# Kernel optimization log

Measured on AMD Instinct MI355X. Metric: run time of the kernel, lower is better.

## Reference

```python
import jax, jax.numpy as jnp
import numpy as np

H, W = 256, 336
FLOW_SCALING = float(max(H, W))  # max(config['loader']['resolution'])
REG_WEIGHT = 0.001               # config['loss']['flow_regul_weight']
B, N = 8, 262144


def setup_inputs() -> dict:
    key = jax.random.key(0)
    k1, k2, k3, k4, k5 = jax.random.split(key, 5)
    # small flow so a reasonable fraction of warped events stays in-bounds
    flow = 0.05 * jax.random.normal(k1, (B, 2, H, W), dtype=jnp.float32)
    ys = jax.random.randint(k2, (B, N), 0, H).astype(jnp.float32)
    xs = jax.random.randint(k3, (B, N), 0, W).astype(jnp.float32)
    ts = jax.random.uniform(k4, (B, N), dtype=jnp.float32)  # normalized timestamps in [0,1]
    pol = jax.random.randint(k5, (B, N), 0, 2)
    # event layout per the code: (ts, y, x, p)
    event_list = jnp.stack([ts, ys, xs, pol.astype(jnp.float32) * 2.0 - 1.0], axis=-1)
    pol_mask = jnp.stack([(pol == 1), (pol == 0)], axis=-1).astype(jnp.float32)  # [B,N,2]
    return {"flow": flow, "event_list": event_list, "pol_mask": pol_mask}


def _get_interpolation(events, event_flow, tref):
    # warped event coords (y, x): [B, N, 2]
    warped = events[:, :, 1:3] + (tref - events[:, :, 0:1]) * event_flow * FLOW_SCALING
    top_y = jnp.floor(warped[:, :, 0:1])
    bot_y = jnp.floor(warped[:, :, 0:1] + 1.0)
    left_x = jnp.floor(warped[:, :, 1:2])
    right_x = jnp.floor(warped[:, :, 1:2] + 1.0)
    # four bilinear corners stacked along event dim -> [B, 4N, 2]
    idx = jnp.concatenate([
        jnp.concatenate([top_y, left_x], -1),
        jnp.concatenate([top_y, right_x], -1),
        jnp.concatenate([bot_y, left_x], -1),
        jnp.concatenate([bot_y, right_x], -1)], axis=1)
    warped4 = jnp.tile(warped, (1, 4, 1))
    weights = jnp.maximum(0.0, 1.0 - jnp.abs(warped4 - idx))
    mask = ((idx[:, :, 0:1] >= 0) & (idx[:, :, 0:1] < H)
            & (idx[:, :, 1:2] >= 0) & (idx[:, :, 1:2] < W)).astype(weights.dtype)
    idx = idx * mask          # unfeasible indices -> 0
    weights = weights * mask  # unfeasible weights -> 0
    flat_idx = (idx[:, :, 0] * W + idx[:, :, 1]).astype(jnp.int32)  # [B, 4N]
    w = jnp.prod(weights, axis=-1, keepdims=True)                    # [B, 4N, 1]
    return flat_idx, w


def _interpolate(flat_idx, weights, polarity_mask):
    # scatter-add bilinear weights into an H*W image, per batch element
    w = (weights * polarity_mask)[:, :, 0]  # [B, 4N]
    return jax.vmap(lambda i, v: jax.ops.segment_sum(v, i, num_segments=H * W))(flat_idx, w)


def reference(flow, event_list, pol_mask):
    pol4 = jnp.tile(pol_mask, (1, 4, 1))              # [B, 4N, 2]
    ts4 = jnp.tile(event_list[:, :, 0:1], (1, 4, 1))  # [B, 4N, 1]
    # gather flow at original event pixel locations
    flow_idx = (event_list[:, :, 1] * W + event_list[:, :, 2]).astype(jnp.int32)  # [B, N]
    flow_flat = flow.reshape(flow.shape[0], 2, -1)
    event_flowy = jnp.take_along_axis(flow_flat[:, 1, :], flow_idx, axis=1)
    event_flowx = jnp.take_along_axis(flow_flat[:, 0, :], flow_idx, axis=1)
    event_flow = jnp.stack([event_flowy, event_flowx], axis=-1)  # [B, N, 2] (y, x)

    loss = jnp.float32(0.0)
    # forward warp (tref=1, avg ts) and backward warp (tref=0, avg 1-ts)
    for tref, tgrad in ((1.0, ts4), (0.0, 1.0 - ts4)):
        idx, wts = _get_interpolation(event_list, event_flow, tref)
        for p in range(2):  # positive / negative polarity
            pm = pol4[:, :, p:p + 1]
            iwe = _interpolate(idx, wts, pm)
            iwe_ts = _interpolate(idx, wts * tgrad, pm)
            loss = loss + jnp.sum((iwe_ts / (iwe + 1e-9)) ** 2)

    # charbonnier flow smoothness
    flow_dx = flow[:, :, :-1, :] - flow[:, :, 1:, :]
    flow_dy = flow[:, :, :, :-1] - flow[:, :, :, 1:]
    smooth = jnp.sum(jnp.sqrt(flow_dx ** 2 + 1e-6)) + jnp.sum(jnp.sqrt(flow_dy ** 2 + 1e-6))
    return loss + REG_WEIGHT * smooth
```

## Files before the change

### kernel.cpp

```cpp
#include <hip/hip_runtime.h>

#define HH 256
#define WW 336
#define HWPIX (HH * WW)
#define BATCH 8
#define NEV 262144
#define NEV_SHIFT 18
#define FLOW_SCALING 336.0f
#define REG_WEIGHT 0.001f

#define BANDS 32
#define BANDSHIFT 3
#define BANDROWS 8
#define NBINS (2 * BATCH * BANDS)
#define CAP 14336
#define GSTRIDE 16

#define BE_THREADS 1024
#define EVPT 2
#define EV_PER_BLOCK (BE_THREADS * EVPT)
#define MAXITEMS 8320

#define HTILE (BANDROWS * WW)
#define NBLK_ACC NBINS

#define GCOUNT_BYTES (NBINS * GSTRIDE * 4)
#define ZERO_BYTES 33024
#define ITEMS_BYTES ((size_t)NBINS * CAP * 8)

__device__ __forceinline__ float wave_reduce_sum(float v) {
    #pragma unroll
    for (int o = 32; o > 0; o >>= 1) v += __shfl_down(v, o, 64);
    return v;
}

__device__ __forceinline__ float charb(float d) { return sqrtf(d * d + 1e-6f); }

__global__ __launch_bounds__(BE_THREADS)
void bin_events(const float* __restrict__ flow,
                const float4* __restrict__ ev,
                unsigned int* __restrict__ gcount,
                uint2* __restrict__ items) {
    __shared__ int lcnt[64];
    __shared__ int loff[64];
    __shared__ int gbase[64];
    __shared__ int stotal;
    __shared__ __align__(16) unsigned long long sval[MAXITEMS];

    int tid = threadIdx.x;
    if (tid < 64) lcnt[tid] = 0;
    __syncthreads();

    int base = blockIdx.x * EV_PER_BLOCK;
    int b = base >> NEV_SHIFT;
    const float* fxp = flow + (size_t)b * 2 * HWPIX;
    const float* fyp = fxp + HWPIX;

    unsigned int pkv[EVPT][2];
    unsigned int hiA[EVPT][2], hiB[EVPT][2];
    int rkA[EVPT][2], rkB[EVPT][2];

    #pragma unroll
    for (int e = 0; e < EVPT; ++e) {
        int bn = base + e * BE_THREADS + tid;
        float4 ee = ev[bn];
        float t = ee.x, y = ee.y, x = ee.z;
        unsigned int p = (ee.w > 0.0f) ? 0u : 1u;

        int iy = (int)y, ix = (int)x;
        int off = iy * WW + ix;
        float fx = fxp[off];
        float fy = fyp[off];

        #pragma unroll
        for (int tr = 0; tr < 2; ++tr) {
            rkA[e][tr] = -1; rkB[e][tr] = -1;
            float tref  = tr ? 0.0f : 1.0f;
            float tg    = tr ? (1.0f - t) : t;
            float dtS = (tref - t) * FLOW_SCALING;
            float wy = fmaf(dtS, fy, y);
            float wx = fmaf(dtS, fx, x);
            if (!(wx > -1.0f && wx < (float)WW)) continue;
            if (!(wy > -1.0f && wy < (float)HH)) continue;

            int ty = (int)floorf(wy);
            int band0 = -1, band1 = -1;
            if (ty >= 0 && ty < HH) band0 = ty >> BANDSHIFT;
            int r1 = ty + 1;
            if (r1 >= 0 && r1 < HH) {
                int bb = r1 >> BANDSHIFT;
                if (bb != band0) band1 = bb;
            }

            unsigned int qx = (unsigned int)(fmaf(wx, 2048.0f, 2048.5f));
            unsigned int qt = (unsigned int)(tg * 2047.0f + 0.5f);
            pkv[e][tr] = (qx << 12) | (qt << 1) | p;

            if (band0 >= 0) {
                float wyrel = wy - (float)(band0 * BANDROWS - 1);
                unsigned int qy = (unsigned int)fmaf(wyrel, 2048.0f, 0.5f);
                int lb = tr * BANDS + band0;
                hiA[e][tr] = qy | ((unsigned int)lb << 16);
                rkA[e][tr] = atomicAdd(&lcnt[lb], 1);
            }
            if (band1 >= 0) {
                float wyrel = wy - (float)(band1 * BANDROWS - 1);
                unsigned int qy = (unsigned int)fmaf(wyrel, 2048.0f, 0.5f);
                int lb = tr * BANDS + band1;
                hiB[e][tr] = qy | ((unsigned int)lb << 16);
                rkB[e][tr] = atomicAdd(&lcnt[lb], 1);
            }
        }
    }
    __syncthreads();

    if (tid < 64) {
        int c  = lcnt[tid];
        int ce = (c + 1) & ~1;
        int xg = ce;
        #pragma unroll
        for (int o = 1; o < 64; o <<= 1) {
            int yv = __shfl_up(xg, o, 64);
            if (tid >= o) xg += yv;
        }
        int lo = xg - ce;
        loff[tid] = lo;
        if (tid == 63) stotal = xg;
        int gbin = ((tid >> 5) * BATCH + b) * BANDS + (tid & 31);
        gbase[tid] = ce > 0 ? (int)atomicAdd(&gcount[gbin * GSTRIDE],
                                             (unsigned int)ce) : 0;
        if (c & 1) {
            unsigned int hi = (15u << 11) | ((unsigned int)tid << 16);
            sval[lo + c] = ((unsigned long long)hi << 32);
        }
    }
    __syncthreads();

    #pragma unroll
    for (int e = 0; e < EVPT; ++e) {
        #pragma unroll
        for (int tr = 0; tr < 2; ++tr) {
            if (rkA[e][tr] >= 0) {
                int lb = (hiA[e][tr] >> 16) & 63;
                sval[loff[lb] + rkA[e][tr]] =
                    (unsigned long long)pkv[e][tr] |
                    ((unsigned long long)hiA[e][tr] << 32);
            }
            if (rkB[e][tr] >= 0) {
                int lb = (hiB[e][tr] >> 16) & 63;
                sval[loff[lb] + rkB[e][tr]] =
                    (unsigned long long)pkv[e][tr] |
                    ((unsigned long long)hiB[e][tr] << 32);
            }
        }
    }
    __syncthreads();

    int total = stotal;
    for (int i = tid * 2; i < total; i += 2 * BE_THREADS) {
        uint4 two = *(const uint4*)&sval[i];
        unsigned int pk0 = two.x, h0 = two.y;
        unsigned int qy0 = h0 & 0xffffu;
        int lb0 = (h0 >> 16) & 63;
        int gs0 = gbase[lb0] + (i - loff[lb0]);
        int gbin0 = ((lb0 >> 5) * BATCH + b) * BANDS + (lb0 & 31);

        if ((i + 1) < total) {
            unsigned int pk1 = two.z, h1 = two.w;
            unsigned int qy1 = h1 & 0xffffu;
            int lb1 = (h1 >> 16) & 63;
            int gs1 = gbase[lb1] + (i + 1 - loff[lb1]);
            if (lb1 == lb0 && (gs0 & 1) == 0 && gs1 < CAP) {
                *(uint4*)(items + (size_t)gbin0 * CAP + gs0) =
                    make_uint4(pk0, qy0, pk1, qy1);
                continue;
            }
            int gbin1 = ((lb1 >> 5) * BATCH + b) * BANDS + (lb1 & 31);
            if (gs1 < CAP) items[(size_t)gbin1 * CAP + gs1] = make_uint2(pk1, qy1);
        }
        if (gs0 < CAP) items[(size_t)gbin0 * CAP + gs0] = make_uint2(pk0, qy0);
    }
}

__device__ __forceinline__ unsigned int pack_w(float w, float tg) {
    unsigned int lo16 = (unsigned int)fmaf(w, 1024.0f, 0.5f);
    unsigned int hi16 = (unsigned int)fmaf(w * tg, 1024.0f, 0.5f);
    return lo16 | (hi16 << 16);
}

__device__ __forceinline__ void accum_item(unsigned int* __restrict__ sA,
                                           unsigned int* __restrict__ sB,
                                           unsigned int pk, unsigned int qy) {
    float wx = (float)(pk >> 12) * (1.0f / 2048.0f) - 1.0f;
    float tg = (float)((pk >> 1) & 2047u) * (1.0f / 2047.0f);
    int p = pk & 1u;

    int rowq = qy >> 11;
    float fy = (float)(qy & 2047u) * (1.0f / 2048.0f);
    int row_top = rowq - 1;

    float lxf = floorf(wx);
    float fxx = wx - lxf;
    int lx = (int)lxf;

    unsigned int* A  = sA + p * HTILE;
    unsigned int* Bb = sB + p * HTILE;

    #pragma unroll
    for (int a = 0; a < 2; ++a) {
        int ry = row_top + a;
        if ((unsigned)ry >= (unsigned)BANDROWS) continue;
        float wrow = a ? fy : (1.0f - fy);
        int rb = ry * WW;
        if (lx >= 0 && lx + 1 < WW) {
            unsigned int pl = pack_w(wrow * (1.0f - fxx), tg);
            unsigned int pr = pack_w(wrow * fxx, tg);
            unsigned long long v =
                (unsigned long long)pl | ((unsigned long long)pr << 32);
            if ((lx & 1) == 0) {
                atomicAdd((unsigned long long*)(A + rb + lx), v);
            } else {
                atomicAdd((unsigned long long*)(Bb + rb + lx - 1), v);
            }
        } else if (lx == -1) {
            atomicAdd(&A[rb], pack_w(wrow * fxx, tg));
        } else if (lx == WW - 1) {
            atomicAdd(&A[rb + lx], pack_w(wrow * (1.0f - fxx), tg));
        }
    }
}

__global__ __launch_bounds__(1024)
void bin_accum(const float* __restrict__ flow,
               const unsigned int* __restrict__ gcount,
               const uint2* __restrict__ items,
               float* __restrict__ loss_acc,
               unsigned int* __restrict__ done_count,
               float* __restrict__ out) {
    __shared__ __align__(16) unsigned int sA[2 * HTILE];
    __shared__ __align__(16) unsigned int sB[2 * HTILE];
    __shared__ float red[16];
    __shared__ int lastflag;

    int band = blockIdx.x;
    int tr   = blockIdx.y;
    int b    = blockIdx.z;
    int tid  = threadIdx.x;
    int lblk = band + 32 * (tr + 2 * b);

    for (int i = tid; i < 2 * HTILE; i += 1024) { sA[i] = 0u; sB[i] = 0u; }
    __syncthreads();

    int gbin = (tr * BATCH + b) * BANDS + band;
    int cnt = min((int)gcount[gbin * GSTRIDE], CAP);
    const uint2* bp = items + (size_t)gbin * CAP;
    const uint4* bp4 = (const uint4*)bp;

    int nquad = cnt >> 2;
    if (tid < nquad) {
        uint4 c0 = bp4[2 * tid];
        uint4 c1 = bp4[2 * tid + 1];
        for (int n = tid + 1024; n < nquad; n += 1024) {
            uint4 d0 = bp4[2 * n];
            uint4 d1 = bp4[2 * n + 1];
            accum_item(sA, sB, c0.x, c0.y);
            accum_item(sA, sB, c0.z, c0.w);
            accum_item(sA, sB, c1.x, c1.y);
            accum_item(sA, sB, c1.z, c1.w);
            c0 = d0; c1 = d1;
        }
        accum_item(sA, sB, c0.x, c0.y);
        accum_item(sA, sB, c0.z, c0.w);
        accum_item(sA, sB, c1.x, c1.y);
        accum_item(sA, sB, c1.z, c1.w);
    }
    int rem = cnt & 3;
    if (tid < rem) {
        uint2 u = bp[nquad * 4 + tid];
        accum_item(sA, sB, u.x, u.y);
    }

    float sm = 0.0f;
    {
        const int N4 = BATCH * HWPIX / 4;
        const int H4 = HWPIX / 4;
        const int W4 = WW / 4;
        for (int i = lblk * 1024 + tid; i < N4; i += NBLK_ACC * 1024) {
            int bb = i / H4, u = i - bb * H4;
            int row = u / W4, c4 = u - row * W4;
            const float4* ch0 = (const float4*)(flow + (size_t)bb * 2 * HWPIX);
            const float4* ch1 = ch0 + H4;
            float4 a0 = ch0[u];
            float4 a1 = ch1[u];
            if (row < HH - 1) {
                float4 d0 = ch0[u + W4];
                float4 d1 = ch1[u + W4];
                sm += charb(a0.x - d0.x) + charb(a0.y - d0.y) +
                      charb(a0.z - d0.z) + charb(a0.w - d0.w) +
                      charb(a1.x - d1.x) + charb(a1.y - d1.y) +
                      charb(a1.z - d1.z) + charb(a1.w - d1.w);
            }
            sm += charb(a0.x - a0.y) + charb(a0.y - a0.z) + charb(a0.z - a0.w) +
                  charb(a1.x - a1.y) + charb(a1.y - a1.z) + charb(a1.z - a1.w);
            if (c4 < W4 - 1) {
                float r0 = ((const float*)ch0)[4 * u + 4];
                float r1 = ((const float*)ch1)[4 * u + 4];
                sm += charb(a0.w - r0) + charb(a1.w - r1);
            }
        }
    }
    __syncthreads();

    float v = 0.0f;
    for (int i = tid; i < 2 * HTILE; i += 1024) {
        int px = i - (i / WW) * WW;
        unsigned int u = sA[i] + (px ? sB[i - 1] : 0u);
        float iwe = (float)(u & 0xffffu);
        float its = (float)(u >> 16);
        float r = its / (iwe + 1.024e-6f);
        v += r * r;
    }
    v = fmaf(sm, REG_WEIGHT, v);
    v = wave_reduce_sum(v);
    if ((tid & 63) == 0) red[tid >> 6] = v;
    __syncthreads();
    if (tid == 0) {
        float r = 0.0f;
        #pragma unroll
        for (int k = 0; k < 16; ++k) r += red[k];
        atomicAdd(loss_acc, r);
        __threadfence();
        unsigned int t = atomicAdd(done_count, 1u);
        lastflag = (t == (unsigned)(NBLK_ACC - 1));
    }
    __syncthreads();

    if (lastflag && tid == 0) {
        *out = atomicAdd(loss_acc, 0.0f);
    }
}

extern "C" void kernel_launch(void* const* d_in, const int* in_sizes, int n_in,
                              void* d_out, int out_size, void* d_ws, size_t ws_size,
                              hipStream_t stream) {
    const float*  flow  = (const float*)d_in[0];
    const float4* ev    = (const float4*)d_in[1];
    float* out = (float*)d_out;

    unsigned int* gcount     = (unsigned int*)d_ws;
    float*        loss_acc   = (float*)((char*)d_ws + GCOUNT_BYTES);
    unsigned int* done_count = (unsigned int*)((char*)d_ws + GCOUNT_BYTES + 4);
    uint2*        items      = (uint2*)((char*)d_ws + GCOUNT_BYTES + 4096);

    hipMemsetAsync(d_ws, 0, ZERO_BYTES, stream);

    int total_ev = BATCH * NEV;
    bin_events<<<total_ev / EV_PER_BLOCK, BE_THREADS, 0, stream>>>(
        flow, ev, gcount, items);

    dim3 g2(BANDS, 2, BATCH);
    bin_accum<<<g2, 1024, 0, stream>>>(flow, gcount, items, loss_acc,
                                       done_count, out);
}
```

Before: 138.3 us.

## Replace band binning with direct global atomic scatter into per-plane accumulators

Drops the two-pass scheme that binned events into row bands and accumulated them in shared memory. Each event now does packed 64-bit atomic adds straight into full-image global accumulator planes, and a separate grid-stride kernel reduces the loss and smoothness term. This removes the binning, prefix-scan and item staging traffic. In exchange it adds a memset of two roughly 11 MB accumulators and relies on global atomics in L2, which have higher latency and can contend where events collide.

```diff
diff --git a/kernel.cpp b/kernel.cpp
--- a/kernel.cpp
+++ b/kernel.cpp
@@ -9,24 +9,18 @@
 #define FLOW_SCALING 336.0f
 #define REG_WEIGHT 0.001f
 
-#define BANDS 32
-#define BANDSHIFT 3
-#define BANDROWS 8
-#define NBINS (2 * BATCH * BANDS)
-#define CAP 14336
-#define GSTRIDE 16
-
-#define BE_THREADS 1024
+#define NPLANE (BATCH * 2 * 2)
+#define ACC_U32 (NPLANE * HWPIX)
+#define ACC_BYTES ((size_t)ACC_U32 * 4)
+
+#define WS_THREADS 1024
 #define EVPT 2
-#define EV_PER_BLOCK (BE_THREADS * EVPT)
-#define MAXITEMS 8320
-
-#define HTILE (BANDROWS * WW)
-#define NBLK_ACC NBINS
-
-#define GCOUNT_BYTES (NBINS * GSTRIDE * 4)
-#define ZERO_BYTES 33024
-#define ITEMS_BYTES ((size_t)NBINS * CAP * 8)
+#define EV_PER_BLOCK (WS_THREADS * EVPT)
+
+#define RL_BLOCKS 512
+#define RL_THREADS 1024
+
+#define ZERO_BYTES (2 * ACC_BYTES + 64)
 
 __device__ __forceinline__ float wave_reduce_sum(float v) {
     #pragma unroll
@@ -36,248 +30,106 @@
 
 __device__ __forceinline__ float charb(float d) { return sqrtf(d * d + 1e-6f); }
 
-__global__ __launch_bounds__(BE_THREADS)
-void bin_events(const float* __restrict__ flow,
-                const float4* __restrict__ ev,
-                unsigned int* __restrict__ gcount,
-                uint2* __restrict__ items) {
-    __shared__ int lcnt[64];
-    __shared__ int loff[64];
-    __shared__ int gbase[64];
-    __shared__ int stotal;
-    __shared__ __align__(16) unsigned long long sval[MAXITEMS];
-
+__device__ __forceinline__ unsigned int pack_w(float w, float tg) {
+    unsigned int lo16 = (unsigned int)fmaf(w, 1024.0f, 0.5f);
+    unsigned int hi16 = (unsigned int)fmaf(w * tg, 1024.0f, 0.5f);
+    return lo16 | (hi16 << 16);
+}
+
+__device__ __forceinline__ void scatter_ev(unsigned int* __restrict__ A,
+                                           unsigned int* __restrict__ B,
+                                           const float* __restrict__ fxp,
+                                           const float* __restrict__ fyp,
+                                           float4 e, int b) {
+    float t = e.x, y = e.y, x = e.z;
+    unsigned int p = (e.w > 0.0f) ? 0u : 1u;
+
+    int off = (int)y * WW + (int)x;
+    float fx = fxp[off];
+    float fy = fyp[off];
+
+    #pragma unroll
+    for (int tr = 0; tr < 2; ++tr) {
+        float tref = tr ? 0.0f : 1.0f;
+        float tg   = tr ? (1.0f - t) : t;
+        float dtS  = (tref - t) * FLOW_SCALING;
+        float wy = fmaf(dtS, fy, y);
+        float wx = fmaf(dtS, fx, x);
+        if (!(wx > -1.0f && wx < (float)WW)) continue;
+        if (!(wy > -1.0f && wy < (float)HH)) continue;
+
+        float tyf = floorf(wy);
+        float lxf = floorf(wx);
+        float fyy = wy - tyf;
+        float fxx = wx - lxf;
+        int ty = (int)tyf;
+        int lx = (int)lxf;
+
+        int pbase = (((b << 1) | tr) << 1 | (int)p) * HWPIX;
+
+        #pragma unroll
+        for (int a = 0; a < 2; ++a) {
+            int ry = ty + a;
+            if ((unsigned)ry >= (unsigned)HH) continue;
+            float wrow = a ? fyy : (1.0f - fyy);
+            int rb = pbase + ry * WW;
+            if (lx >= 0 && lx + 1 < WW) {
+                unsigned int pl = pack_w(wrow * (1.0f - fxx), tg);
+                unsigned int pr = pack_w(wrow * fxx, tg);
+                unsigned long long v =
+                    (unsigned long long)pl | ((unsigned long long)pr << 32);
+                if ((lx & 1) == 0) {
+                    atomicAdd((unsigned long long*)(A + rb + lx), v);
+                } else {
+                    atomicAdd((unsigned long long*)(B + rb + lx - 1), v);
+                }
+            } else if (lx == -1) {
+                atomicAdd(&A[rb], pack_w(wrow * fxx, tg));
+            } else if (lx == WW - 1) {
+                atomicAdd(&A[rb + lx], pack_w(wrow * (1.0f - fxx), tg));
+            }
+        }
+    }
+}
+
+__global__ __launch_bounds__(WS_THREADS)
+void warp_scatter(const float* __restrict__ flow,
+                  const float4* __restrict__ ev,
+                  unsigned int* __restrict__ A,
+                  unsigned int* __restrict__ B) {
     int tid = threadIdx.x;
-    if (tid < 64) lcnt[tid] = 0;
-    __syncthreads();
-
     int base = blockIdx.x * EV_PER_BLOCK;
     int b = base >> NEV_SHIFT;
     const float* fxp = flow + (size_t)b * 2 * HWPIX;
     const float* fyp = fxp + HWPIX;
 
-    unsigned int pkv[EVPT][2];
-    unsigned int hiA[EVPT][2], hiB[EVPT][2];
-    int rkA[EVPT][2], rkB[EVPT][2];
-
-    #pragma unroll
-    for (int e = 0; e < EVPT; ++e) {
-        int bn = base + e * BE_THREADS + tid;
-        float4 ee = ev[bn];
-        float t = ee.x, y = ee.y, x = ee.z;
-        unsigned int p = (ee.w > 0.0f) ? 0u : 1u;
-
-        int iy = (int)y, ix = (int)x;
-        int off = iy * WW + ix;
-        float fx = fxp[off];
-        float fy = fyp[off];
-
-        #pragma unroll
-        for (int tr = 0; tr < 2; ++tr) {
-            rkA[e][tr] = -1; rkB[e][tr] = -1;
-            float tref  = tr ? 0.0f : 1.0f;
-            float tg    = tr ? (1.0f - t) : t;
-            float dtS = (tref - t) * FLOW_SCALING;
-            float wy = fmaf(dtS, fy, y);
-            float wx = fmaf(dtS, fx, x);
-            if (!(wx > -1.0f && wx < (float)WW)) continue;
-            if (!(wy > -1.0f && wy < (float)HH)) continue;
-
-            int ty = (int)floorf(wy);
-            int band0 = -1, band1 = -1;
-            if (ty >= 0 && ty < HH) band0 = ty >> BANDSHIFT;
-            int r1 = ty + 1;
-            if (r1 >= 0 && r1 < HH) {
-                int bb = r1 >> BANDSHIFT;
-                if (bb != band0) band1 = bb;
-            }
-
-            unsigned int qx = (unsigned int)(fmaf(wx, 2048.0f, 2048.5f));
-            unsigned int qt = (unsigned int)(tg * 2047.0f + 0.5f);
-            pkv[e][tr] = (qx << 12) | (qt << 1) | p;
-
-            if (band0 >= 0) {
-                float wyrel = wy - (float)(band0 * BANDROWS - 1);
-                unsigned int qy = (unsigned int)fmaf(wyrel, 2048.0f, 0.5f);
-                int lb = tr * BANDS + band0;
-                hiA[e][tr] = qy | ((unsigned int)lb << 16);
-                rkA[e][tr] = atomicAdd(&lcnt[lb], 1);
-            }
-            if (band1 >= 0) {
-                float wyrel = wy - (float)(band1 * BANDROWS - 1);
-                unsigned int qy = (unsigned int)fmaf(wyrel, 2048.0f, 0.5f);
-                int lb = tr * BANDS + band1;
-                hiB[e][tr] = qy | ((unsigned int)lb << 16);
-                rkB[e][tr] = atomicAdd(&lcnt[lb], 1);
-            }
-        }
-    }
-    __syncthreads();
-
-    if (tid < 64) {
-        int c  = lcnt[tid];
-        int ce = (c + 1) & ~1;
-        int xg = ce;
-        #pragma unroll
-        for (int o = 1; o < 64; o <<= 1) {
-            int yv = __shfl_up(xg, o, 64);
-            if (tid >= o) xg += yv;
-        }
-        int lo = xg - ce;
-        loff[tid] = lo;
-        if (tid == 63) stotal = xg;
-        int gbin = ((tid >> 5) * BATCH + b) * BANDS + (tid & 31);
-        gbase[tid] = ce > 0 ? (int)atomicAdd(&gcount[gbin * GSTRIDE],
-                                             (unsigned int)ce) : 0;
-        if (c & 1) {
-            unsigned int hi = (15u << 11) | ((unsigned int)tid << 16);
-            sval[lo + c] = ((unsigned long long)hi << 32);
-        }
-    }
-    __syncthreads();
-
-    #pragma unroll
-    for (int e = 0; e < EVPT; ++e) {
-        #pragma unroll
-        for (int tr = 0; tr < 2; ++tr) {
-            if (rkA[e][tr] >= 0) {
-                int lb = (hiA[e][tr] >> 16) & 63;
-                sval[loff[lb] + rkA[e][tr]] =
-                    (unsigned long long)pkv[e][tr] |
-                    ((unsigned long long)hiA[e][tr] << 32);
-            }
-            if (rkB[e][tr] >= 0) {
-                int lb = (hiB[e][tr] >> 16) & 63;
-                sval[loff[lb] + rkB[e][tr]] =
-                    (unsigned long long)pkv[e][tr] |
-                    ((unsigned long long)hiB[e][tr] << 32);
-            }
-        }
-    }
-    __syncthreads();
-
-    int total = stotal;
-    for (int i = tid * 2; i < total; i += 2 * BE_THREADS) {
-        uint4 two = *(const uint4*)&sval[i];
-        unsigned int pk0 = two.x, h0 = two.y;
-        unsigned int qy0 = h0 & 0xffffu;
-        int lb0 = (h0 >> 16) & 63;
-        int gs0 = gbase[lb0] + (i - loff[lb0]);
-        int gbin0 = ((lb0 >> 5) * BATCH + b) * BANDS + (lb0 & 31);
-
-        if ((i + 1) < total) {
-            unsigned int pk1 = two.z, h1 = two.w;
-            unsigned int qy1 = h1 & 0xffffu;
-            int lb1 = (h1 >> 16) & 63;
-            int gs1 = gbase[lb1] + (i + 1 - loff[lb1]);
-            if (lb1 == lb0 && (gs0 & 1) == 0 && gs1 < CAP) {
-                *(uint4*)(items + (size_t)gbin0 * CAP + gs0) =
-                    make_uint4(pk0, qy0, pk1, qy1);
-                continue;
-            }
-            int gbin1 = ((lb1 >> 5) * BATCH + b) * BANDS + (lb1 & 31);
-            if (gs1 < CAP) items[(size_t)gbin1 * CAP + gs1] = make_uint2(pk1, qy1);
-        }
-        if (gs0 < CAP) items[(size_t)gbin0 * CAP + gs0] = make_uint2(pk0, qy0);
-    }
-}
-
-__device__ __forceinline__ unsigned int pack_w(float w, float tg) {
-    unsigned int lo16 = (unsigned int)fmaf(w, 1024.0f, 0.5f);
-    unsigned int hi16 = (unsigned int)fmaf(w * tg, 1024.0f, 0.5f);
-    return lo16 | (hi16 << 16);
-}
-
-__device__ __forceinline__ void accum_item(unsigned int* __restrict__ sA,
-                                           unsigned int* __restrict__ sB,
-                                           unsigned int pk, unsigned int qy) {
-    float wx = (float)(pk >> 12) * (1.0f / 2048.0f) - 1.0f;
-    float tg = (float)((pk >> 1) & 2047u) * (1.0f / 2047.0f);
-    int p = pk & 1u;
-
-    int rowq = qy >> 11;
-    float fy = (float)(qy & 2047u) * (1.0f / 2048.0f);
-    int row_top = rowq - 1;
-
-    float lxf = floorf(wx);
-    float fxx = wx - lxf;
-    int lx = (int)lxf;
-
-    unsigned int* A  = sA + p * HTILE;
-    unsigned int* Bb = sB + p * HTILE;
-
-    #pragma unroll
-    for (int a = 0; a < 2; ++a) {
-        int ry = row_top + a;
-        if ((unsigned)ry >= (unsigned)BANDROWS) continue;
-        float wrow = a ? fy : (1.0f - fy);
-        int rb = ry * WW;
-        if (lx >= 0 && lx + 1 < WW) {
-            unsigned int pl = pack_w(wrow * (1.0f - fxx), tg);
-            unsigned int pr = pack_w(wrow * fxx, tg);
-            unsigned long long v =
-                (unsigned long long)pl | ((unsigned long long)pr << 32);
-            if ((lx & 1) == 0) {
-                atomicAdd((unsigned long long*)(A + rb + lx), v);
-            } else {
-                atomicAdd((unsigned long long*)(Bb + rb + lx - 1), v);
-            }
-        } else if (lx == -1) {
-            atomicAdd(&A[rb], pack_w(wrow * fxx, tg));
-        } else if (lx == WW - 1) {
-            atomicAdd(&A[rb + lx], pack_w(wrow * (1.0f - fxx), tg));
-        }
-    }
-}
-
-__global__ __launch_bounds__(1024)
-void bin_accum(const float* __restrict__ flow,
-               const unsigned int* __restrict__ gcount,
-               const uint2* __restrict__ items,
-               float* __restrict__ loss_acc,
-               unsigned int* __restrict__ done_count,
-               float* __restrict__ out) {
-    __shared__ __align__(16) unsigned int sA[2 * HTILE];
-    __shared__ __align__(16) unsigned int sB[2 * HTILE];
+    float4 e0 = ev[base + tid];
+    float4 e1 = ev[base + WS_THREADS + tid];
+
+    scatter_ev(A, B, fxp, fyp, e0, b);
+    scatter_ev(A, B, fxp, fyp, e1, b);
+}
+
+__global__ __launch_bounds__(RL_THREADS)
+void reduce_loss(const unsigned int* __restrict__ A,
+                 const unsigned int* __restrict__ B,
+                 const float* __restrict__ flow,
+                 float* __restrict__ loss_acc,
+                 unsigned int* __restrict__ done_count,
+                 float* __restrict__ out) {
     __shared__ float red[16];
     __shared__ int lastflag;
-
-    int band = blockIdx.x;
-    int tr   = blockIdx.y;
-    int b    = blockIdx.z;
-    int tid  = threadIdx.x;
-    int lblk = band + 32 * (tr + 2 * b);
-
-    for (int i = tid; i < 2 * HTILE; i += 1024) { sA[i] = 0u; sB[i] = 0u; }
-    __syncthreads();
-
-    int gbin = (tr * BATCH + b) * BANDS + band;
-    int cnt = min((int)gcount[gbin * GSTRIDE], CAP);
-    const uint2* bp = items + (size_t)gbin * CAP;
-    const uint4* bp4 = (const uint4*)bp;
-
-    int nquad = cnt >> 2;
-    if (tid < nquad) {
-        uint4 c0 = bp4[2 * tid];
-        uint4 c1 = bp4[2 * tid + 1];
-        for (int n = tid + 1024; n < nquad; n += 1024) {
-            uint4 d0 = bp4[2 * n];
-            uint4 d1 = bp4[2 * n + 1];
-            accum_item(sA, sB, c0.x, c0.y);
-            accum_item(sA, sB, c0.z, c0.w);
-            accum_item(sA, sB, c1.x, c1.y);
-            accum_item(sA, sB, c1.z, c1.w);
-            c0 = d0; c1 = d1;
-        }
-        accum_item(sA, sB, c0.x, c0.y);
-        accum_item(sA, sB, c0.z, c0.w);
-        accum_item(sA, sB, c1.x, c1.y);
-        accum_item(sA, sB, c1.z, c1.w);
-    }
-    int rem = cnt & 3;
-    if (tid < rem) {
-        uint2 u = bp[nquad * 4 + tid];
-        accum_item(sA, sB, u.x, u.y);
+    int tid = threadIdx.x;
+    int gid = blockIdx.x * RL_THREADS + tid;
+
+    float v = 0.0f;
+    for (int i = gid; i < ACC_U32; i += RL_BLOCKS * RL_THREADS) {
+        int px = i - (i / WW) * WW;
+        unsigned int u = A[i] + (px ? B[i - 1] : 0u);
+        float iwe = (float)(u & 0xffffu);
+        float its = (float)(u >> 16);
+        float r = its / (iwe + 1.024e-6f);
+        v += r * r;
     }
 
     float sm = 0.0f;
@@ -285,7 +137,7 @@
         const int N4 = BATCH * HWPIX / 4;
         const int H4 = HWPIX / 4;
         const int W4 = WW / 4;
-        for (int i = lblk * 1024 + tid; i < N4; i += NBLK_ACC * 1024) {
+        for (int i = gid; i < N4; i += RL_BLOCKS * RL_THREADS) {
             int bb = i / H4, u = i - bb * H4;
             int row = u / W4, c4 = u - row * W4;
             const float4* ch0 = (const float4*)(flow + (size_t)bb * 2 * HWPIX);
@@ -309,17 +161,7 @@
             }
         }
     }
-    __syncthreads();
-
-    float v = 0.0f;
-    for (int i = tid; i < 2 * HTILE; i += 1024) {
-        int px = i - (i / WW) * WW;
-        unsigned int u = sA[i] + (px ? sB[i - 1] : 0u);
-        float iwe = (float)(u & 0xffffu);
-        float its = (float)(u >> 16);
-        float r = its / (iwe + 1.024e-6f);
-        v += r * r;
-    }
+
     v = fmaf(sm, REG_WEIGHT, v);
     v = wave_reduce_sum(v);
     if ((tid & 63) == 0) red[tid >> 6] = v;
@@ -331,7 +173,7 @@
         atomicAdd(loss_acc, r);
         __threadfence();
         unsigned int t = atomicAdd(done_count, 1u);
-        lastflag = (t == (unsigned)(NBLK_ACC - 1));
+        lastflag = (t == (unsigned)(RL_BLOCKS - 1));
     }
     __syncthreads();
 
@@ -347,18 +189,17 @@
     const float4* ev    = (const float4*)d_in[1];
     float* out = (float*)d_out;
 
-    unsigned int* gcount     = (unsigned int*)d_ws;
-    float*        loss_acc   = (float*)((char*)d_ws + GCOUNT_BYTES);
-    unsigned int* done_count = (unsigned int*)((char*)d_ws + GCOUNT_BYTES + 4);
-    uint2*        items      = (uint2*)((char*)d_ws + GCOUNT_BYTES + 4096);
+    unsigned int* A          = (unsigned int*)d_ws;
+    unsigned int* B          = (unsigned int*)((char*)d_ws + ACC_BYTES);
+    float*        loss_acc   = (float*)((char*)d_ws + 2 * ACC_BYTES);
+    unsigned int* done_count = (unsigned int*)((char*)d_ws + 2 * ACC_BYTES + 4);
 
     hipMemsetAsync(d_ws, 0, ZERO_BYTES, stream);
 
     int total_ev = BATCH * NEV;
-    bin_events<<<total_ev / EV_PER_BLOCK, BE_THREADS, 0, stream>>>(
-        flow, ev, gcount, items);
-
-    dim3 g2(BANDS, 2, BATCH);
-    bin_accum<<<g2, 1024, 0, stream>>>(flow, gcount, items, loss_acc,
-                                       done_count, out);
-}
+    warp_scatter<<<total_ev / EV_PER_BLOCK, WS_THREADS, 0, stream>>>(
+        flow, ev, A, B);
+
+    reduce_loss<<<RL_BLOCKS, RL_THREADS, 0, stream>>>(
+        A, B, flow, loss_acc, done_count, out);
+}
```

New measurement: 448.9 us. 3.25x slower.
